# Performance work log

Hardware: AMD Instinct MI355X
Metric: run time of the kernel (lower is better)

Reference implementation:

```python
import jax, jax.numpy as jnp
import numpy as np

B = 8192      # batch
T = 8         # obs_len
E = 256       # feature_dim
M = 20        # num_modes
NH = 4        # attention heads
HD = E // NH  # head dim
FS = 12       # future_steps
LN_EPS = 1e-5


def setup_inputs() -> dict:
    key = jax.random.key(0)
    ks = jax.random.split(key, 32)
    s = 0.05
    def n(i, shape):
        return jax.random.normal(ks[i], shape, jnp.float32) * s
    return {
        "observed_trajectory": jax.random.normal(ks[0], (B, T, 2), jnp.float32),
        # 2-layer LSTM (torch gate order i,f,g,o)
        "w_ih0": n(1, (4 * E, 2)), "w_hh0": n(2, (4 * E, E)),
        "b_ih0": n(3, (4 * E,)), "b_hh0": n(4, (4 * E,)),
        "w_ih1": n(5, (4 * E, E)), "w_hh1": n(6, (4 * E, E)),
        "b_ih1": n(7, (4 * E,)), "b_hh1": n(8, (4 * E,)),
        # 20 MHA modules, weights stacked over mode axis
        "in_proj_w": n(9, (M, 3 * E, E)), "in_proj_b": n(10, (M, 3 * E)),
        "out_w": n(11, (M, E, E)), "out_b": n(12, (M, E)),
        # FFN: LN -> Linear(256,1024) -> ReLU -> Linear(1024,256) -> LN
        "ln1_g": jnp.ones((E,)), "ln1_b": jnp.zeros((E,)),
        "ffn_w1": n(13, (1024, E)), "ffn_b1": n(14, (1024,)),
        "ffn_w2": n(15, (E, 1024)), "ffn_b2": n(16, (E,)),
        "ln2_g": jnp.ones((E,)), "ln2_b": jnp.zeros((E,)),
        # decoder MLP
        "dec_w1": n(17, (512, E)), "dec_b1": n(18, (512,)),
        "dec_w2": n(19, (FS * 2, 512)), "dec_b2": n(20, (FS * 2,)),
        # scorer MLP
        "sc_w1": n(21, (128, E)), "sc_b1": n(22, (128,)),
        "sc_w2": n(23, (1, 128)), "sc_b2": n(24, (1,)),
    }


def _lstm_layer(xs, w_ih, w_hh, b_ih, b_hh):
    # xs: (T, B, in_dim) -> (ys (T,B,E), h_T (B,E))
    bb = xs.shape[1]
    h0 = jnp.zeros((bb, E), xs.dtype)
    c0 = jnp.zeros((bb, E), xs.dtype)
    def step(carry, x):
        h, c = carry
        g = x @ w_ih.T + h @ w_hh.T + b_ih + b_hh
        i, f, gg, o = jnp.split(g, 4, axis=-1)
        c = jax.nn.sigmoid(f) * c + jax.nn.sigmoid(i) * jnp.tanh(gg)
        h = jax.nn.sigmoid(o) * jnp.tanh(c)
        return (h, c), h
    (h_t, _), ys = jax.lax.scan(step, (h0, c0), xs)
    return ys, h_t


def _ln(x, g, b):
    m = jnp.mean(x, -1, keepdims=True)
    v = jnp.mean((x - m) ** 2, -1, keepdims=True)
    return (x - m) * jax.lax.rsqrt(v + LN_EPS) * g + b


def _forward(observed_trajectory, w_ih0, w_hh0, b_ih0, b_hh0,
             w_ih1, w_hh1, b_ih1, b_hh1,
             in_proj_w, in_proj_b, out_w, out_b,
             ln1_g, ln1_b, ffn_w1, ffn_b1, ffn_w2, ffn_b2, ln2_g, ln2_b,
             dec_w1, dec_b1, dec_w2, dec_b2,
             sc_w1, sc_b1, sc_w2, sc_b2):
    bsz = observed_trajectory.shape[0]
    # --- TrajectoryEncoder: 2-layer LSTM, take last-step output of layer 2 ---
    xs = jnp.transpose(observed_trajectory, (1, 0, 2))  # (T, B, 2)
    ys0, _ = _lstm_layer(xs, w_ih0, w_hh0, b_ih0, b_hh0)
    _, emb = _lstm_layer(ys0, w_ih1, w_hh1, b_ih1, b_hh1)  # (B, E)

    # --- MultiModalTransformer: 20 MHA modules on seq_len=1 (fused over modes) ---
    # query == key == value == emb. Dropout is eval-mode identity.
    qkv = jnp.einsum('be,mfe->bmf', emb, in_proj_w) + in_proj_b  # (B, M, 3E)
    q, k, v = jnp.split(qkv, 3, axis=-1)
    q = q.reshape(bsz, M, NH, HD)
    k = k.reshape(bsz, M, NH, HD)
    v = v.reshape(bsz, M, NH, HD)
    # kv length is 1 -> softmax over a single score is identically 1
    scores = jnp.sum(q * k, -1, keepdims=True) / jnp.sqrt(jnp.float32(HD))  # (B,M,NH,1)
    attn = jax.nn.softmax(scores, axis=-1)
    ctx = (attn * v).reshape(bsz, M, E)
    attn_out = jnp.einsum('bmf,mof->bmo', ctx, out_w) + out_b  # (B, M, E)
    # FFN (no residual in original module)
    h = _ln(attn_out, ln1_g, ln1_b)
    h = jax.nn.relu(h @ ffn_w1.T + ffn_b1)
    h = h @ ffn_w2.T + ffn_b2
    mm_emb = _ln(h, ln2_g, ln2_b)  # (B, M, E)

    # --- TrajectoryDecoder ---
    last_pos = observed_trajectory[:, -1, :]  # (B, 2)
    d = jax.nn.elu(mm_emb @ dec_w1.T + dec_b1)
    deltas = (d @ dec_w2.T + dec_b2).reshape(bsz, M, FS, 2)
    predictions = deltas + last_pos[:, None, None, :]

    # --- ModeScorer ---
    s = jax.nn.elu(mm_emb @ sc_w1.T + sc_b1)
    scores_out = (s @ sc_w2.T + sc_b2)[..., 0]  # (B, M)
    return predictions, scores_out


def reference(observed_trajectory, w_ih0, w_hh0, b_ih0, b_hh0,
              w_ih1, w_hh1, b_ih1, b_hh1,
              in_proj_w, in_proj_b, out_w, out_b,
              ln1_g, ln1_b, ffn_w1, ffn_b1, ffn_w2, ffn_b2, ln2_g, ln2_b,
              dec_w1, dec_b1, dec_w2, dec_b2,
              sc_w1, sc_b1, sc_w2, sc_b2):
    return _forward(observed_trajectory, w_ih0, w_hh0, b_ih0, b_hh0,
                    w_ih1, w_hh1, b_ih1, b_hh1,
                    in_proj_w, in_proj_b, out_w, out_b,
                    ln1_g, ln1_b, ffn_w1, ffn_b1, ffn_w2, ffn_b2, ln2_g, ln2_b,
                    dec_w1, dec_b1, dec_w2, dec_b2,
                    sc_w1, sc_b1, sc_w2, sc_b2)
```

## Files before the change

### kernel.cpp

```cpp
#include <hip/hip_runtime.h>
#include <math.h>


typedef float4 f4;
typedef unsigned int u32;
typedef unsigned short u16;
typedef __attribute__((ext_vector_type(16))) float f32x16;
typedef __attribute__((ext_vector_type(8)))  short s16x8;

__device__ __forceinline__ float sigm(float x){ return 1.0f/(1.0f + __expf(-x)); }
__device__ __forceinline__ float tanhfast(float x){ return 2.0f*sigm(2.0f*x) - 1.0f; }
__device__ __forceinline__ float eluf(float x){ return x > 0.f ? x : __expf(x) - 1.0f; }
__device__ __forceinline__ u16 f2bf(float x){
  u32 u = __float_as_uint(x);
  return (u16)((u + 0x7FFFu + ((u>>16)&1u)) >> 16);
}
__device__ __forceinline__ float bf2f(u16 h){ return __uint_as_float(((u32)h)<<16); }


#define LSTR 264

__global__ __launch_bounds__(256, 4)
void w2c_kernel(const float* __restrict__ out_w, const float* __restrict__ ipw,
                float* __restrict__ W2c)
{
  __shared__ float As[16][68];
  __shared__ float Bs2[16][68];
  const int tid = threadIdx.x;
  const int m = blockIdx.y;
  const int o0 = (blockIdx.x >> 2) * 64, e0 = (blockIdx.x & 3) * 64;
  const int trow = tid >> 4, tcol = tid & 15;
  const float* Ap = out_w + (size_t)m * 65536;
  const float* Bp = ipw + ((size_t)m * 768 + 512) * 256;
  float acc[16];
#pragma unroll
  for (int z = 0; z < 16; ++z) acc[z] = 0.f;
  for (int kb = 0; kb < 256; kb += 16) {
    { int row = tid >> 2, ko = (tid & 3) * 4;
      f4 v = *(const f4*)(Ap + (size_t)(o0+row)*256 + kb + ko);
      As[ko+0][row]=v.x; As[ko+1][row]=v.y; As[ko+2][row]=v.z; As[ko+3][row]=v.w; }
    { int k = tid >> 4, eo = (tid & 15) * 4;
      *(f4*)&Bs2[k][eo] = *(const f4*)(Bp + (size_t)(kb+k)*256 + e0 + eo); }
    __syncthreads();
#pragma unroll
    for (int k = 0; k < 16; ++k) {
      f4 a4 = *(const f4*)&As[k][trow*4];
      f4 b4 = *(const f4*)&Bs2[k][tcol*4];
      acc[0]+=a4.x*b4.x; acc[1]+=a4.x*b4.y; acc[2]+=a4.x*b4.z; acc[3]+=a4.x*b4.w;
      acc[4]+=a4.y*b4.x; acc[5]+=a4.y*b4.y; acc[6]+=a4.y*b4.z; acc[7]+=a4.y*b4.w;
      acc[8]+=a4.z*b4.x; acc[9]+=a4.z*b4.y; acc[10]+=a4.z*b4.z; acc[11]+=a4.z*b4.w;
      acc[12]+=a4.w*b4.x; acc[13]+=a4.w*b4.y; acc[14]+=a4.w*b4.z; acc[15]+=a4.w*b4.w;
    }
    __syncthreads();
  }
#pragma unroll
  for (int i = 0; i < 4; ++i)
    *(f4*)&W2c[((size_t)m*256 + o0 + trow*4 + i)*256 + e0 + tcol*4] =
        make_float4(acc[i*4+0], acc[i*4+1], acc[i*4+2], acc[i*4+3]);
}

__global__ void b2c_kernel(const float* __restrict__ out_w, const float* __restrict__ out_b,
                           const float* __restrict__ ipb, float* __restrict__ b2c)
{
  __shared__ float pb[256];
  const int m = blockIdx.x, o = threadIdx.x;
  pb[o] = ipb[(size_t)m*768 + 512 + o];
  __syncthreads();
  const float* wr = out_w + ((size_t)m*256 + o)*256;
  float acc = out_b[(size_t)m*256 + o];
  for (int f = 0; f < 256; f += 4) {
    f4 w = *(const f4*)&wr[f];
    acc += w.x*pb[f] + w.y*pb[f+1] + w.z*pb[f+2] + w.w*pb[f+3];
  }
  b2c[(size_t)m*256 + o] = acc;
}

__device__ __forceinline__ void cvt_seg(const float* __restrict__ src, u16* __restrict__ dst,
                                        int Creal, int lognks, int g)
{
  const int l = g & 63;
  const int cks = g >> 6;
  const int ks = cks & ((1 << lognks) - 1);
  const int ct = cks >> lognks;
  const int c = ct*32 + (l & 31);
  const int K = 16 << lognks;
  const int k = ks*16 + ((l >> 5) * 8);
  s16x8 r;
  if (c < Creal) {
    const float* s = src + (size_t)c * K + k;
    f4 v0 = *(const f4*)s;
    f4 v1 = *(const f4*)(s + 4);
    r[0]=(short)f2bf(v0.x); r[1]=(short)f2bf(v0.y); r[2]=(short)f2bf(v0.z); r[3]=(short)f2bf(v0.w);
    r[4]=(short)f2bf(v1.x); r[5]=(short)f2bf(v1.y); r[6]=(short)f2bf(v1.z); r[7]=(short)f2bf(v1.w);
  } else {
#pragma unroll
    for (int j = 0; j < 8; ++j) r[j] = 0;
  }
  *(s16x8*)(dst + (size_t)g * 8) = r;
}

__global__ __launch_bounds__(256)
void wcvt_all(const float* __restrict__ whh0, const float* __restrict__ wih1,
              const float* __restrict__ whh1, const float* __restrict__ W2c,
              const float* __restrict__ ffn1, const float* __restrict__ ffn2,
              const float* __restrict__ dec1, const float* __restrict__ dec2,
              const float* __restrict__ sc1,  u16* __restrict__ dst)
{
  int g = blockIdx.x * 256 + threadIdx.x;
  if      (g <  32768) cvt_seg(whh0, dst + 0,       1024, 4, g);
  else if (g <  65536) cvt_seg(wih1, dst + 262144,  1024, 4, g - 32768);
  else if (g <  98304) cvt_seg(whh1, dst + 524288,  1024, 4, g - 65536);
  else if (g < 262144) cvt_seg(W2c,  dst + 786432,  5120, 4, g - 98304);
  else if (g < 294912) cvt_seg(ffn1, dst + 2097152, 1024, 4, g - 262144);
  else if (g < 327680) cvt_seg(ffn2, dst + 2359296,  256, 6, g - 294912);
  else if (g < 344064) cvt_seg(dec1, dst + 2621440,  512, 4, g - 327680);
  else if (g < 346112) cvt_seg(dec2, dst + 2752512,   24, 5, g - 344064);
  else if (g < 350208) cvt_seg(sc1,  dst + 2768896,  128, 4, g - 346112);
}

__global__ __launch_bounds__(512, 2)
void lstm_fused(const u16* __restrict__ whh0f, const u16* __restrict__ wih1f,
                const u16* __restrict__ whh1f, const float* __restrict__ w_ih0,
                const float* __restrict__ b_ih0, const float* __restrict__ b_hh0,
                const float* __restrict__ b_ih1, const float* __restrict__ b_hh1,
                const float* __restrict__ obs, u16* __restrict__ emb)
{
  __shared__ u16 h0s[32 * LSTR];
  __shared__ u16 h1s[32 * LSTR];
  __shared__ float obs_s[512];
  const int tid = threadIdx.x;
  const int lane = tid & 63, w = tid >> 6;
  const int col = lane & 31, hi = lane >> 5;
  const int r0 = blockIdx.x * 32;
  obs_s[tid] = obs[(size_t)r0 * 16 + tid];

  float bs0[4], bs1[4], xw0[4], xw1[4];
#pragma unroll
  for (int g = 0; g < 4; ++g) {
    const int cg = g*256 + w*32 + col;
    bs0[g] = b_ih0[cg] + b_hh0[cg];
    bs1[g] = b_ih1[cg] + b_hh1[cg];
    xw0[g] = w_ih0[2*cg];
    xw1[g] = w_ih0[2*cg + 1];
  }
  float c0v[16], c1v[16];
#pragma unroll
  for (int r = 0; r < 16; ++r) { c0v[r] = 0.f; c1v[r] = 0.f; }

  f32x16 za;
#pragma unroll
  for (int i = 0; i < 16; ++i) za[i] = 0.f;

  __syncthreads();
#pragma unroll
  for (int r = 0; r < 16; ++r) {
    const int row = (r&3) + 8*(r>>2) + 4*hi;
    const float x0 = obs_s[row*16], x1 = obs_s[row*16 + 1];
    const float gi = bs0[0] + x0*xw0[0] + x1*xw1[0];
    const float gg = bs0[2] + x0*xw0[2] + x1*xw1[2];
    const float go = bs0[3] + x0*xw0[3] + x1*xw1[3];
    const float cn = sigm(gi)*tanhfast(gg);
    c0v[r] = cn;
    h0s[row*LSTR + w*32 + col] = f2bf(sigm(go)*tanhfast(cn));
  }
  __syncthreads();

  for (int t = 0; t < 8; ++t) {
    f32x16 aL1[4], aL0[4];
#pragma unroll
    for (int g = 0; g < 4; ++g) { aL1[g] = za; aL0[g] = za; }
    if (t > 0) {
#pragma unroll 2
      for (int ks = 0; ks < 16; ++ks) {
        s16x8 a0 = *(const s16x8*)(h0s + col*LSTR + ks*16 + hi*8);
        s16x8 a1 = *(const s16x8*)(h1s + col*LSTR + ks*16 + hi*8);
#pragma unroll
        for (int g = 0; g < 4; ++g) {
          const size_t fo = ((size_t)((g*8 + w)*16 + ks)*64 + lane)*8;
          s16x8 b0 = *(const s16x8*)(wih1f + fo);
          aL1[g] = __builtin_amdgcn_mfma_f32_32x32x16_bf16(a0, b0, aL1[g], 0, 0, 0);
          s16x8 b1 = *(const s16x8*)(whh1f + fo);
          aL1[g] = __builtin_amdgcn_mfma_f32_32x32x16_bf16(a1, b1, aL1[g], 0, 0, 0);
          s16x8 b2 = *(const s16x8*)(whh0f + fo);
          aL0[g] = __builtin_amdgcn_mfma_f32_32x32x16_bf16(a0, b2, aL0[g], 0, 0, 0);
        }
      }
    } else {
#pragma unroll 2
      for (int ks = 0; ks < 16; ++ks) {
        s16x8 a0 = *(const s16x8*)(h0s + col*LSTR + ks*16 + hi*8);
#pragma unroll
        for (int g = 0; g < 4; ++g) {
          const size_t fo = ((size_t)((g*8 + w)*16 + ks)*64 + lane)*8;
          s16x8 b0 = *(const s16x8*)(wih1f + fo);
          aL1[g] = __builtin_amdgcn_mfma_f32_32x32x16_bf16(a0, b0, aL1[g], 0, 0, 0);
          s16x8 b2 = *(const s16x8*)(whh0f + fo);
          aL0[g] = __builtin_amdgcn_mfma_f32_32x32x16_bf16(a0, b2, aL0[g], 0, 0, 0);
        }
      }
    }
    __syncthreads();
#pragma unroll
    for (int r = 0; r < 16; ++r) {
      const int row = (r&3) + 8*(r>>2) + 4*hi;
      const float gi = aL1[0][r] + bs1[0];
      const float gf = aL1[1][r] + bs1[1];
      const float gg = aL1[2][r] + bs1[2];
      const float go = aL1[3][r] + bs1[3];
      const float cn = sigm(gf)*c1v[r] + sigm(gi)*tanhfast(gg);
      c1v[r] = cn;
      h1s[row*LSTR + w*32 + col] = f2bf(sigm(go)*tanhfast(cn));
    }
    if (t < 7) {
#pragma unroll
      for (int r = 0; r < 16; ++r) {
        const int row = (r&3) + 8*(r>>2) + 4*hi;
        const float x0 = obs_s[row*16 + 2*(t+1)], x1 = obs_s[row*16 + 2*(t+1) + 1];
        const float gi = aL0[0][r] + bs0[0] + x0*xw0[0] + x1*xw1[0];
        const float gf = aL0[1][r] + bs0[1] + x0*xw0[1] + x1*xw1[1];
        const float gg = aL0[2][r] + bs0[2] + x0*xw0[2] + x1*xw1[2];
        const float go = aL0[3][r] + bs0[3] + x0*xw0[3] + x1*xw1[3];
        const float cn = sigm(gf)*c0v[r] + sigm(gi)*tanhfast(gg);
        c0v[r] = cn;
        h0s[row*LSTR + w*32 + col] = f2bf(sigm(go)*tanhfast(cn));
      }
    }
    __syncthreads();
  }
#pragma unroll
  for (int kk = 0; kk < 2; ++kk) {
    const int gi2 = tid + kk*512;
    const int row = gi2 >> 5, grp = gi2 & 31;
    *(s16x8*)(emb + (size_t)(r0 + row)*256 + grp*8) = *(const s16x8*)(h1s + row*LSTR + grp*8);
  }
}

__device__ __forceinline__ void gemmP(const u16* As, const u16* __restrict__ Bf,
                                      f32x16 acc[2], int ct, int lane)
{
  const int col = lane & 31, hi = lane >> 5;
  __builtin_amdgcn_s_setprio(1);
#pragma unroll 4
  for (int ks = 0; ks < 16; ++ks) {
    s16x8 b = *(const s16x8*)(Bf + ((size_t)(ct*16 + ks)*64 + lane)*8);
#pragma unroll
    for (int i = 0; i < 2; ++i) {
      s16x8 a = *(const s16x8*)(As + (i*32 + col)*LSTR + ks*16 + hi*8);
      acc[i] = __builtin_amdgcn_mfma_f32_32x32x16_bf16(a, b, acc[i], 0, 0, 0);
    }
  }
  __builtin_amdgcn_s_setprio(0);
}

__device__ __forceinline__ void gemmF2(const u16* As, const u16* __restrict__ Bf,
                                       f32x16 acc[2], int c4, int ct, int lane)
{
  const int col = lane & 31, hi = lane >> 5;
  __builtin_amdgcn_s_setprio(1);
#pragma unroll 4
  for (int ks = 0; ks < 16; ++ks) {
    s16x8 b = *(const s16x8*)(Bf + ((size_t)(ct*64 + c4*16 + ks)*64 + lane)*8);
#pragma unroll
    for (int i = 0; i < 2; ++i) {
      s16x8 a = *(const s16x8*)(As + (i*32 + col)*LSTR + ks*16 + hi*8);
      acc[i] = __builtin_amdgcn_mfma_f32_32x32x16_bf16(a, b, acc[i], 0, 0, 0);
    }
  }
  __builtin_amdgcn_s_setprio(0);
}

template<int ACT>
__device__ __forceinline__ void epiP(f32x16 acc[2], const float* __restrict__ bias,
                                     u16* Ys, int ct, int lane)
{
  const int col = lane & 31, hi = lane >> 5, cg = ct*32 + col;
  const float bv = bias[cg];
#pragma unroll
  for (int i = 0; i < 2; ++i)
#pragma unroll
    for (int r = 0; r < 16; ++r) {
      float v = acc[i][r] + bv;
      if (ACT == 1) v = fmaxf(v, 0.f);
      else if (ACT == 2) v = eluf(v);
      const int row = i*32 + (r&3) + 8*(r>>2) + 4*hi;
      Ys[row*LSTR + cg] = f2bf(v);
    }
}

__device__ __forceinline__ void lnp(const u16* In, u16* Out,
    const float* __restrict__ g, const float* __restrict__ b, int tid)
{
  const int lane = tid & 63, w = tid >> 6;
  f4 gv = *(const f4*)&g[lane*4];
  f4 bv = *(const f4*)&b[lane*4];
#pragma unroll
  for (int i = 0; i < 8; ++i) {
    const int row = w*8 + i;
    ushort4 uv = *(const ushort4*)(In + row*LSTR + lane*4);
    float v0 = bf2f(uv.x), v1 = bf2f(uv.y), v2 = bf2f(uv.z), v3 = bf2f(uv.w);
    float s  = v0 + v1 + v2 + v3;
    float ss = v0*v0 + v1*v1 + v2*v2 + v3*v3;
#pragma unroll
    for (int d = 1; d < 64; d <<= 1) { s += __shfl_xor(s, d); ss += __shfl_xor(ss, d); }
    const float mean = s * (1.f/256.f);
    const float rs = rsqrtf(ss * (1.f/256.f) - mean*mean + 1e-5f);
    ushort4 o;
    o.x = f2bf((v0 - mean)*rs*gv.x + bv.x);
    o.y = f2bf((v1 - mean)*rs*gv.y + bv.y);
    o.z = f2bf((v2 - mean)*rs*gv.z + bv.z);
    o.w = f2bf((v3 - mean)*rs*gv.w + bv.w);
    *(ushort4*)(Out + row*LSTR + lane*4) = o;
  }
}

__global__ __launch_bounds__(512, 4)
void mode_stack(const u16* __restrict__ emb, const u16* __restrict__ W2cf,
  const float* __restrict__ b2c,
  const float* __restrict__ ln1_g, const float* __restrict__ ln1_b,
  const u16* __restrict__ ffn1f, const float* __restrict__ ffn_b1,
  const u16* __restrict__ ffn2f, const float* __restrict__ ffn_b2,
  const float* __restrict__ ln2_g, const float* __restrict__ ln2_b,
  const u16* __restrict__ dec1f, const float* __restrict__ dec_b1,
  const u16* __restrict__ dec2f, const float* __restrict__ dec_b2,
  const u16* __restrict__ sc1f,  const float* __restrict__ sc_b1,
  const float* __restrict__ sc_w2, const float* __restrict__ sc_b2,
  const float* __restrict__ obs, float* __restrict__ pred, float* __restrict__ score)
{
  __shared__ u16 Xs[64 * LSTR];
  __shared__ u16 Ys[64 * LSTR];
  __shared__ float obs_ls[128];
  const int tid = threadIdx.x;
  const int lane = tid & 63, w = tid >> 6;
  const int ct = w;
  const int col = lane & 31, hi = lane >> 5;
  const int r0 = blockIdx.x * 64;
  const int m  = blockIdx.y;

  f32x16 za;
#pragma unroll
  for (int i = 0; i < 16; ++i) za[i] = 0.f;

#pragma unroll
  for (int kk = 0; kk < 4; ++kk) {
    const int gi2 = tid + kk*512;
    const int row = gi2 >> 5, grp = gi2 & 31;
    *(s16x8*)(Xs + row*LSTR + grp*8) = *(const s16x8*)(emb + (size_t)(r0 + row)*256 + grp*8);
  }
  if (tid < 128) obs_ls[tid] = obs[(size_t)(r0 + (tid >> 1))*16 + 14 + (tid & 1)];
  __syncthreads();

  {
    f32x16 acc[2]; acc[0] = za; acc[1] = za;
    gemmP(Xs, W2cf + (size_t)m*65536, acc, ct, lane);
    epiP<0>(acc, b2c + m*256, Ys, ct, lane);
  }
  __syncthreads();
  lnp(Ys, Xs, ln1_g, ln1_b, tid);
  __syncthreads();

  f32x16 h2[2]; h2[0] = za; h2[1] = za;
  for (int c4 = 0; c4 < 4; ++c4) {
    f32x16 tacc[2]; tacc[0] = za; tacc[1] = za;
    gemmP(Xs, ffn1f + (size_t)c4*65536, tacc, ct, lane);
    epiP<1>(tacc, ffn_b1 + c4*256, Ys, ct, lane);
    __syncthreads();
    gemmF2(Ys, ffn2f, h2, c4, ct, lane);
    __syncthreads();
  }
  epiP<0>(h2, ffn_b2, Ys, ct, lane);
  __syncthreads();
  lnp(Ys, Xs, ln2_g, ln2_b, tid);
  __syncthreads();

  f32x16 dv[2]; dv[0] = za; dv[1] = za;
  for (int c2 = 0; c2 < 2; ++c2) {
    f32x16 tacc[2]; tacc[0] = za; tacc[1] = za;
    gemmP(Xs, dec1f + (size_t)c2*65536, tacc, ct, lane);
    epiP<2>(tacc, dec_b1 + c2*256, Ys, ct, lane);
    __syncthreads();
    if (w == 0) {
#pragma unroll 4
      for (int ks = 0; ks < 16; ++ks) {
        s16x8 b = *(const s16x8*)(dec2f + ((size_t)(c2*16 + ks)*64 + lane)*8);
#pragma unroll
        for (int i = 0; i < 2; ++i) {
          s16x8 a = *(const s16x8*)(Ys + (i*32 + col)*LSTR + ks*16 + hi*8);
          dv[i] = __builtin_amdgcn_mfma_f32_32x32x16_bf16(a, b, dv[i], 0, 0, 0);
        }
      }
    }
    __syncthreads();
  }
  if (w == 0 && col < 24) {
    const float db = dec_b2[col];
#pragma unroll
    for (int i = 0; i < 2; ++i)
#pragma unroll
      for (int r = 0; r < 16; ++r) {
        const int row = i*32 + (r&3) + 8*(r>>2) + 4*hi;
        const float lp = obs_ls[row*2 + (col & 1)];
        pred[((size_t)(r0 + row)*20 + m)*24 + col] = dv[i][r] + db + lp;
      }
  }

  if (w < 4) {
    f32x16 sacc[2]; sacc[0] = za; sacc[1] = za;
    gemmP(Xs, sc1f, sacc, ct, lane);
    epiP<2>(sacc, sc_b1, Ys, ct, lane);
  }
  __syncthreads();
  {
    const float scb2 = sc_b2[0];
    const float2 w2v = *(const float2*)&sc_w2[lane*2];
#pragma unroll
    for (int i = 0; i < 8; ++i) {
      const int row = w*8 + i;
      u32 pv = *(const u32*)(Ys + row*LSTR + lane*2);
      float part = bf2f((u16)(pv & 0xFFFF))*w2v.x + bf2f((u16)(pv >> 16))*w2v.y;
#pragma unroll
      for (int d = 1; d < 64; d <<= 1) part += __shfl_xor(part, d);
      if (lane == 0) score[(size_t)(r0 + row)*20 + m] = part + scb2;
    }
  }
}

extern "C" void kernel_launch(void* const* d_in, const int* in_sizes, int n_in,
                              void* d_out, int out_size, void* d_ws, size_t ws_size,
                              hipStream_t stream)
{
  (void)in_sizes; (void)n_in; (void)out_size; (void)ws_size;
  const float* obs    = (const float*)d_in[0];
  const float* w_ih0  = (const float*)d_in[1];
  const float* w_hh0  = (const float*)d_in[2];
  const float* b_ih0  = (const float*)d_in[3];
  const float* b_hh0  = (const float*)d_in[4];
  const float* w_ih1  = (const float*)d_in[5];
  const float* w_hh1  = (const float*)d_in[6];
  const float* b_ih1  = (const float*)d_in[7];
  const float* b_hh1  = (const float*)d_in[8];
  const float* ipw    = (const float*)d_in[9];
  const float* ipb    = (const float*)d_in[10];
  const float* out_w  = (const float*)d_in[11];
  const float* out_b  = (const float*)d_in[12];
  const float* ln1_g  = (const float*)d_in[13];
  const float* ln1_b  = (const float*)d_in[14];
  const float* ffn_w1 = (const float*)d_in[15];
  const float* ffn_b1 = (const float*)d_in[16];
  const float* ffn_w2 = (const float*)d_in[17];
  const float* ffn_b2 = (const float*)d_in[18];
  const float* ln2_g  = (const float*)d_in[19];
  const float* ln2_b  = (const float*)d_in[20];
  const float* dec_w1 = (const float*)d_in[21];
  const float* dec_b1 = (const float*)d_in[22];
  const float* dec_w2 = (const float*)d_in[23];
  const float* dec_b2 = (const float*)d_in[24];
  const float* sc_w1  = (const float*)d_in[25];
  const float* sc_b1  = (const float*)d_in[26];
  const float* sc_w2  = (const float*)d_in[27];
  const float* sc_b2  = (const float*)d_in[28];

  float* outp   = (float*)d_out;
  float* pred   = outp;
  float* scoreo = outp + (size_t)8192*20*24;

  float* wsf   = (float*)d_ws;
  float* W2c   = wsf;
  float* b2cp  = wsf + 1310720;
  u16*   wsh   = (u16*)(wsf + 1315840);
  u16* whh0f = wsh + 0;
  u16* wih1f = wsh + 262144;
  u16* whh1f = wsh + 524288;
  u16* W2cf  = wsh + 786432;
  u16* ffn1f = wsh + 2097152;
  u16* ffn2f = wsh + 2359296;
  u16* dec1f = wsh + 2621440;
  u16* dec2f = wsh + 2752512;
  u16* sc1f  = wsh + 2768896;
  u16* emb   = wsh + 2801664;

  w2c_kernel<<<dim3(16, 20), 256, 0, stream>>>(out_w, ipw, W2c);
  b2c_kernel<<<20, 256, 0, stream>>>(out_w, out_b, ipb, b2cp);
  wcvt_all<<<1368, 256, 0, stream>>>(w_hh0, w_ih1, w_hh1, W2c, ffn_w1, ffn_w2,
                                     dec_w1, dec_w2, sc_w1, wsh);
  lstm_fused<<<256, 512, 0, stream>>>(whh0f, wih1f, whh1f, w_ih0, b_ih0, b_hh0,
                                      b_ih1, b_hh1, obs, emb);
  mode_stack<<<dim3(128, 20), 512, 0, stream>>>(emb, W2cf, b2cp,
      ln1_g, ln1_b, ffn1f, ffn_b1, ffn2f, ffn_b2, ln2_g, ln2_b,
      dec1f, dec_b1, dec2f, dec_b2, sc1f, sc_b1, sc_w2, sc_b2,
      obs, pred, scoreo);
}
```

Measured before the change: 776.2 us.

## Restructure LSTM kernel to 64-row blocks with serialized per-layer GEMMs

The fused LSTM kernel now processes 64 batch rows per block with 1024 threads. Sixteen waves split as 8 column tiles by 2 row halves, so waves sharing a column tile read the same weight fragments. The layer-1 and layer-0 recurrent GEMMs now run one after the other through a single 4-accumulator set instead of 8 live accumulators, which cuts register pressure. Biases and input weights are staged in LDS instead of registers. The cost is an extra barrier per timestep, serialized GEMM phases, and only 128 blocks, which may leave half the CUs idle during this kernel.

Measured after the change: 1.081 ms. 1.39x slower.

```diff
diff --git a/kernel.cpp b/kernel.cpp
--- a/kernel.cpp
+++ b/kernel.cpp
@@ -118,31 +118,31 @@
   else if (g < 350208) cvt_seg(sc1,  dst + 2768896,  128, 4, g - 346112);
 }
 
-__global__ __launch_bounds__(512, 2)
+__global__ __launch_bounds__(1024, 4)
 void lstm_fused(const u16* __restrict__ whh0f, const u16* __restrict__ wih1f,
                 const u16* __restrict__ whh1f, const float* __restrict__ w_ih0,
                 const float* __restrict__ b_ih0, const float* __restrict__ b_hh0,
                 const float* __restrict__ b_ih1, const float* __restrict__ b_hh1,
                 const float* __restrict__ obs, u16* __restrict__ emb)
 {
-  __shared__ u16 h0s[32 * LSTR];
-  __shared__ u16 h1s[32 * LSTR];
-  __shared__ float obs_s[512];
+  __shared__ u16 h0s[64 * LSTR];
+  __shared__ u16 h1s[64 * LSTR];
+  __shared__ float obs_s[1024];
+  __shared__ float bs0_ls[1024], bs1_ls[1024], xw0_ls[1024], xw1_ls[1024];
   const int tid = threadIdx.x;
   const int lane = tid & 63, w = tid >> 6;
+  const int ct = w & 7, rh = w >> 3;
   const int col = lane & 31, hi = lane >> 5;
-  const int r0 = blockIdx.x * 32;
-  obs_s[tid] = obs[(size_t)r0 * 16 + tid];
-
-  float bs0[4], bs1[4], xw0[4], xw1[4];
-#pragma unroll
-  for (int g = 0; g < 4; ++g) {
-    const int cg = g*256 + w*32 + col;
-    bs0[g] = b_ih0[cg] + b_hh0[cg];
-    bs1[g] = b_ih1[cg] + b_hh1[cg];
-    xw0[g] = w_ih0[2*cg];
-    xw1[g] = w_ih0[2*cg + 1];
-  }
+  const int r0 = blockIdx.x * 64;
+  obs_s[tid]  = obs[(size_t)r0*16 + tid];
+  bs0_ls[tid] = b_ih0[tid] + b_hh0[tid];
+  bs1_ls[tid] = b_ih1[tid] + b_hh1[tid];
+  xw0_ls[tid] = w_ih0[2*tid];
+  xw1_ls[tid] = w_ih0[2*tid + 1];
+
+  const int cg = ct*32 + col;
+  const int arow = (rh*32 + col)*LSTR;
+
   float c0v[16], c1v[16];
 #pragma unroll
   for (int r = 0; r < 16; ++r) { c0v[r] = 0.f; c1v[r] = 0.f; }
@@ -152,84 +152,102 @@
   for (int i = 0; i < 16; ++i) za[i] = 0.f;
 
   __syncthreads();
-#pragma unroll
-  for (int r = 0; r < 16; ++r) {
-    const int row = (r&3) + 8*(r>>2) + 4*hi;
-    const float x0 = obs_s[row*16], x1 = obs_s[row*16 + 1];
-    const float gi = bs0[0] + x0*xw0[0] + x1*xw1[0];
-    const float gg = bs0[2] + x0*xw0[2] + x1*xw1[2];
-    const float go = bs0[3] + x0*xw0[3] + x1*xw1[3];
-    const float cn = sigm(gi)*tanhfast(gg);
-    c0v[r] = cn;
-    h0s[row*LSTR + w*32 + col] = f2bf(sigm(go)*tanhfast(cn));
+  {
+    const float b0i = bs0_ls[cg],     b0g = bs0_ls[512+cg], b0o = bs0_ls[768+cg];
+    const float wi0 = xw0_ls[cg],     wi1 = xw1_ls[cg];
+    const float wg0 = xw0_ls[512+cg], wg1 = xw1_ls[512+cg];
+    const float wo0 = xw0_ls[768+cg], wo1 = xw1_ls[768+cg];
+#pragma unroll
+    for (int r = 0; r < 16; ++r) {
+      const int row = rh*32 + (r&3) + 8*(r>>2) + 4*hi;
+      const float x0 = obs_s[row*16], x1 = obs_s[row*16 + 1];
+      const float cn = sigm(b0i + x0*wi0 + x1*wi1) * tanhfast(b0g + x0*wg0 + x1*wg1);
+      c0v[r] = cn;
+      h0s[row*LSTR + cg] = f2bf(sigm(b0o + x0*wo0 + x1*wo1) * tanhfast(cn));
+    }
   }
   __syncthreads();
 
   for (int t = 0; t < 8; ++t) {
-    f32x16 aL1[4], aL0[4];
-#pragma unroll
-    for (int g = 0; g < 4; ++g) { aL1[g] = za; aL0[g] = za; }
+    f32x16 acc[4];
+#pragma unroll
+    for (int g = 0; g < 4; ++g) acc[g] = za;
     if (t > 0) {
 #pragma unroll 2
       for (int ks = 0; ks < 16; ++ks) {
-        s16x8 a0 = *(const s16x8*)(h0s + col*LSTR + ks*16 + hi*8);
-        s16x8 a1 = *(const s16x8*)(h1s + col*LSTR + ks*16 + hi*8);
+        s16x8 a0 = *(const s16x8*)(h0s + arow + ks*16 + hi*8);
+        s16x8 a1 = *(const s16x8*)(h1s + arow + ks*16 + hi*8);
 #pragma unroll
         for (int g = 0; g < 4; ++g) {
-          const size_t fo = ((size_t)((g*8 + w)*16 + ks)*64 + lane)*8;
+          const size_t fo = ((size_t)((g*8 + ct)*16 + ks)*64 + lane)*8;
           s16x8 b0 = *(const s16x8*)(wih1f + fo);
-          aL1[g] = __builtin_amdgcn_mfma_f32_32x32x16_bf16(a0, b0, aL1[g], 0, 0, 0);
+          acc[g] = __builtin_amdgcn_mfma_f32_32x32x16_bf16(a0, b0, acc[g], 0, 0, 0);
           s16x8 b1 = *(const s16x8*)(whh1f + fo);
-          aL1[g] = __builtin_amdgcn_mfma_f32_32x32x16_bf16(a1, b1, aL1[g], 0, 0, 0);
-          s16x8 b2 = *(const s16x8*)(whh0f + fo);
-          aL0[g] = __builtin_amdgcn_mfma_f32_32x32x16_bf16(a0, b2, aL0[g], 0, 0, 0);
+          acc[g] = __builtin_amdgcn_mfma_f32_32x32x16_bf16(a1, b1, acc[g], 0, 0, 0);
         }
       }
     } else {
-#pragma unroll 2
+#pragma unroll 4
       for (int ks = 0; ks < 16; ++ks) {
-        s16x8 a0 = *(const s16x8*)(h0s + col*LSTR + ks*16 + hi*8);
+        s16x8 a0 = *(const s16x8*)(h0s + arow + ks*16 + hi*8);
 #pragma unroll
         for (int g = 0; g < 4; ++g) {
-          const size_t fo = ((size_t)((g*8 + w)*16 + ks)*64 + lane)*8;
-          s16x8 b0 = *(const s16x8*)(wih1f + fo);
-          aL1[g] = __builtin_amdgcn_mfma_f32_32x32x16_bf16(a0, b0, aL1[g], 0, 0, 0);
-          s16x8 b2 = *(const s16x8*)(whh0f + fo);
-          aL0[g] = __builtin_amdgcn_mfma_f32_32x32x16_bf16(a0, b2, aL0[g], 0, 0, 0);
+          s16x8 b0 = *(const s16x8*)(wih1f + ((size_t)((g*8 + ct)*16 + ks)*64 + lane)*8);
+          acc[g] = __builtin_amdgcn_mfma_f32_32x32x16_bf16(a0, b0, acc[g], 0, 0, 0);
         }
       }
     }
     __syncthreads();
-#pragma unroll
-    for (int r = 0; r < 16; ++r) {
-      const int row = (r&3) + 8*(r>>2) + 4*hi;
-      const float gi = aL1[0][r] + bs1[0];
-      const float gf = aL1[1][r] + bs1[1];
-      const float gg = aL1[2][r] + bs1[2];
-      const float go = aL1[3][r] + bs1[3];
-      const float cn = sigm(gf)*c1v[r] + sigm(gi)*tanhfast(gg);
-      c1v[r] = cn;
-      h1s[row*LSTR + w*32 + col] = f2bf(sigm(go)*tanhfast(cn));
+    {
+      const float b1i = bs1_ls[cg],       b1f = bs1_ls[256+cg];
+      const float b1g = bs1_ls[512+cg],   b1o = bs1_ls[768+cg];
+#pragma unroll
+      for (int r = 0; r < 16; ++r) {
+        const int row = rh*32 + (r&3) + 8*(r>>2) + 4*hi;
+        const float cn = sigm(acc[1][r] + b1f)*c1v[r]
+                       + sigm(acc[0][r] + b1i)*tanhfast(acc[2][r] + b1g);
+        c1v[r] = cn;
+        h1s[row*LSTR + cg] = f2bf(sigm(acc[3][r] + b1o)*tanhfast(cn));
+      }
     }
     if (t < 7) {
 #pragma unroll
-      for (int r = 0; r < 16; ++r) {
-        const int row = (r&3) + 8*(r>>2) + 4*hi;
-        const float x0 = obs_s[row*16 + 2*(t+1)], x1 = obs_s[row*16 + 2*(t+1) + 1];
-        const float gi = aL0[0][r] + bs0[0] + x0*xw0[0] + x1*xw1[0];
-        const float gf = aL0[1][r] + bs0[1] + x0*xw0[1] + x1*xw1[1];
-        const float gg = aL0[2][r] + bs0[2] + x0*xw0[2] + x1*xw1[2];
-        const float go = aL0[3][r] + bs0[3] + x0*xw0[3] + x1*xw1[3];
-        const float cn = sigm(gf)*c0v[r] + sigm(gi)*tanhfast(gg);
-        c0v[r] = cn;
-        h0s[row*LSTR + w*32 + col] = f2bf(sigm(go)*tanhfast(cn));
-      }
-    }
-    __syncthreads();
-  }
+      for (int g = 0; g < 4; ++g) acc[g] = za;
+#pragma unroll 4
+      for (int ks = 0; ks < 16; ++ks) {
+        s16x8 a0 = *(const s16x8*)(h0s + arow + ks*16 + hi*8);
+#pragma unroll
+        for (int g = 0; g < 4; ++g) {
+          s16x8 b2 = *(const s16x8*)(whh0f + ((size_t)((g*8 + ct)*16 + ks)*64 + lane)*8);
+          acc[g] = __builtin_amdgcn_mfma_f32_32x32x16_bf16(a0, b2, acc[g], 0, 0, 0);
+        }
+      }
+      __syncthreads();
+      {
+        const float b0i = bs0_ls[cg],     b0f = bs0_ls[256+cg];
+        const float b0g = bs0_ls[512+cg], b0o = bs0_ls[768+cg];
+        const float wi0 = xw0_ls[cg],     wi1 = xw1_ls[cg];
+        const float wf0 = xw0_ls[256+cg], wf1 = xw1_ls[256+cg];
+        const float wg0 = xw0_ls[512+cg], wg1 = xw1_ls[512+cg];
+        const float wo0 = xw0_ls[768+cg], wo1 = xw1_ls[768+cg];
+#pragma unroll
+        for (int r = 0; r < 16; ++r) {
+          const int row = rh*32 + (r&3) + 8*(r>>2) + 4*hi;
+          const float x0 = obs_s[row*16 + 2*(t+1)], x1 = obs_s[row*16 + 2*(t+1) + 1];
+          const float cn = sigm(acc[1][r] + b0f + x0*wf0 + x1*wf1)*c0v[r]
+                         + sigm(acc[0][r] + b0i + x0*wi0 + x1*wi1)
+                           * tanhfast(acc[2][r] + b0g + x0*wg0 + x1*wg1);
+          c0v[r] = cn;
+          h0s[row*LSTR + cg] = f2bf(sigm(acc[3][r] + b0o + x0*wo0 + x1*wo1)*tanhfast(cn));
+        }
+      }
+      __syncthreads();
+    }
+  }
+  __syncthreads();
 #pragma unroll
   for (int kk = 0; kk < 2; ++kk) {
-    const int gi2 = tid + kk*512;
+    const int gi2 = tid + kk*1024;
     const int row = gi2 >> 5, grp = gi2 & 31;
     *(s16x8*)(emb + (size_t)(r0 + row)*256 + grp*8) = *(const s16x8*)(h1s + row*LSTR + grp*8);
   }
@@ -482,8 +500,8 @@
   b2c_kernel<<<20, 256, 0, stream>>>(out_w, out_b, ipb, b2cp);
   wcvt_all<<<1368, 256, 0, stream>>>(w_hh0, w_ih1, w_hh1, W2c, ffn_w1, ffn_w2,
                                      dec_w1, dec_w2, sc_w1, wsh);
-  lstm_fused<<<256, 512, 0, stream>>>(whh0f, wih1f, whh1f, w_ih0, b_ih0, b_hh0,
-                                      b_ih1, b_hh1, obs, emb);
+  lstm_fused<<<128, 1024, 0, stream>>>(whh0f, wih1f, whh1f, w_ih0, b_ih0, b_hh0,
+                                       b_ih1, b_hh1, obs, emb);
   mode_stack<<<dim3(128, 20), 512, 0, stream>>>(emb, W2cf, b2cp,
       ln1_g, ln1_b, ffn1f, ffn_b1, ffn2f, ffn_b2, ln2_g, ln2_b,
       dec1f, dec_b1, dec2f, dec_b2, sc1f, sc_b1, sc_w2, sc_b2,
```
